# Kernel optimization log

Hardware: AMD Instinct MI355X
Metric: run time of the kernel (lower is better)

## Reference

```python
import jax, jax.numpy as jnp
import numpy as np

N_VOLS, N_PARTS = 4, 8          # hard-coded in GL.forward
B = N_VOLS * N_PARTS            # asserted batch size = 32
DIM, HID, PROJ = 8192, 4096, 256
TEMP = 0.1
BN_EPS = 1e-5


def setup_inputs() -> dict:
    key = jax.random.key(0)
    k = jax.random.split(key, 5)
    s1 = 1.0 / np.sqrt(DIM)
    s2 = 1.0 / np.sqrt(HID)
    return {
        "x": jax.random.normal(k[0], (B, DIM), jnp.float32),
        "W1": jax.random.uniform(k[1], (DIM, HID), jnp.float32, -s1, s1),
        "b1": jax.random.uniform(k[2], (HID,), jnp.float32, -s1, s1),
        "gamma": jnp.ones((HID,), jnp.float32),
        "beta": jnp.zeros((HID,), jnp.float32),
        "W2": jax.random.uniform(k[3], (HID, PROJ), jnp.float32, -s2, s2),
        "b2": jax.random.uniform(k[4], (PROJ,), jnp.float32, -s2, s2),
    }


def _gl_loss(proj):
    # F.normalize(p=2, dim=-1); CosineSimilarity on unit vectors == dot product
    p = proj / jnp.linalg.norm(proj, axis=-1, keepdims=True)
    sims = (p @ p.T) / TEMP                       # [B, B]
    idx = jnp.arange(B)
    # pos_index(i) = {i % n_parts + v * n_parts} -> same part id; includes i itself
    pos_mask = (idx[:, None] % N_PARTS) == (idx[None, :] % N_PARTS)  # [B, B], 4 per row
    neg_mask = ~pos_mask                                             # 28 per row
    E = jnp.exp(sims)                              # original uses raw exp (no max-shift)
    row_neg = jnp.sum(jnp.where(neg_mask, E, 0.0), axis=1)    # sum_j exp(s[i, neg_j])
    ET = E.T                                        # ET[i, p] = exp(s[p, i])
    col_neg = jnp.sum(jnp.where(neg_mask, ET, 0.0), axis=1)   # sum_j exp(s[neg_j, i])
    t1 = -jnp.log(E / (E + row_neg[:, None]))      # row-direction term per (i, pos)
    t2 = -jnp.log(ET / (ET + col_neg[:, None]))    # column-direction term per (i, pos)
    per_row = jnp.sum(jnp.where(pos_mask, t1 + t2, 0.0), axis=1) / N_VOLS
    return jnp.sum(per_row) / (B * 2)


def reference(x, W1, b1, gamma, beta, W2, b2):
    # projector MLP: Linear -> BatchNorm1d (training stats) -> ReLU -> Linear
    h = x @ W1 + b1
    mu = jnp.mean(h, axis=0)
    var = jnp.var(h, axis=0)                       # biased variance, BN training mode
    h = gamma * (h - mu) * jax.lax.rsqrt(var + BN_EPS) + beta
    h = jax.nn.relu(h)
    proj = h @ W2 + b2                             # [B, PROJ]
    return _gl_loss(proj)
```

## Files before the change

### kernel.cpp

```cpp
#include <hip/hip_runtime.h>

#define DIM   8192
#define HID   4096
#define PROJ  256
#define NB    32
#define KSPLIT 8
#define KCH   (DIM / KSPLIT)

typedef __attribute__((ext_vector_type(8))) short bf16x8;
typedef __attribute__((ext_vector_type(4))) float f32x4;

__device__ __forceinline__ float bf2f(unsigned short u) {
    return __uint_as_float(((unsigned)u) << 16);
}
__device__ __forceinline__ unsigned short f2bf(float f) {
    unsigned u = __float_as_uint(f);
    u += 0x7fffu + ((u >> 16) & 1u);
    return (unsigned short)(u >> 16);
}
__device__ __forceinline__ unsigned pk2(float a, float b) {
    return (unsigned)f2bf(a) | ((unsigned)f2bf(b) << 16);
}

__device__ __forceinline__ bool detect_bf16(const unsigned* __restrict__ xw, int lane) {
    unsigned v = xw[lane];
    int e = (int)((v >> 7) & 0xffu);
    bool pl = (e >= 100 && e <= 135);
    unsigned long long b = __ballot(pl);
    return __popcll(b) >= 32;
}

__global__ __launch_bounds__(256, 2) void gemm1_kernel(
    const void* __restrict__ xv, const void* __restrict__ W1v,
    float* __restrict__ hpart)
{
    __shared__ unsigned short wt[2 * 32 * 66];
    const int t  = threadIdx.x;
    const int nb = blockIdx.x & 63;
    const int kc = blockIdx.x >> 6;
    const int n0 = nb * 64;
    const int k0 = kc * KCH;

    const bool isbf = detect_bf16((const unsigned*)xv, t & 63);
    const unsigned short* xu  = (const unsigned short*)xv;
    const float*          xf  = (const float*)xv;
    const unsigned short* W1u = (const unsigned short*)W1v;
    const float*          W1f = (const float*)W1v;

    const int lane = t & 63;
    const int w    = t >> 6;
    const int g    = lane >> 4;
    const int ln   = lane & 15;
    const int wr   = t >> 3;
    const int wc   = (t & 7) * 8;

    auto loadW1 = [&](int kt) -> uint4 {
        const int base = (k0 + kt * 32 + wr) * HID + n0 + wc;
        if (isbf) return *(const uint4*)(W1u + base);
        float4 f0 = *(const float4*)(W1f + base);
        float4 f1 = *(const float4*)(W1f + base + 4);
        return make_uint4(pk2(f0.x, f0.y), pk2(f0.z, f0.w),
                          pk2(f1.x, f1.y), pk2(f1.z, f1.w));
    };
    auto storeTile = [&](int buf, uint4 v) {
        unsigned* dst = (unsigned*)&wt[buf * 2112 + wr * 66 + wc];
        dst[0] = v.x; dst[1] = v.y; dst[2] = v.z; dst[3] = v.w;
    };
    auto loadA = [&](int kt, int mt) -> bf16x8 {
        const int base = (mt * 16 + ln) * DIM + k0 + kt * 32 + g * 8;
        if (isbf) return *(const bf16x8*)(xu + base);
        float4 f0 = *(const float4*)(xf + base);
        float4 f1 = *(const float4*)(xf + base + 4);
        union { uint4 u; bf16x8 v; } c;
        c.u = make_uint4(pk2(f0.x, f0.y), pk2(f0.z, f0.w),
                         pk2(f1.x, f1.y), pk2(f1.z, f1.w));
        return c.v;
    };

    storeTile(0, loadW1(0));
    bf16x8 a0 = loadA(0, 0);
    bf16x8 a1 = loadA(0, 1);
    uint4  p0 = loadW1(1);
    __syncthreads();

    f32x4 acc0 = {0.f, 0.f, 0.f, 0.f};
    f32x4 acc1 = {0.f, 0.f, 0.f, 0.f};
    const int bco = w * 16 + ln;

    for (int kt = 0; kt < 32; ++kt) {
        const int cur = kt & 1;
        uint4 p1 = p0;
        if (kt + 2 < 32) p1 = loadW1(kt + 2);
        bf16x8 na0 = a0, na1 = a1;
        if (kt + 1 < 32) { na0 = loadA(kt + 1, 0); na1 = loadA(kt + 1, 1); }

        bf16x8 b;
        const unsigned short* wpb = wt + cur * 2112 + g * 528 + bco;
        #pragma unroll
        for (int j = 0; j < 8; ++j) b[j] = (short)wpb[j * 66];

        acc0 = __builtin_amdgcn_mfma_f32_16x16x32_bf16(a0, b, acc0, 0, 0, 0);
        acc1 = __builtin_amdgcn_mfma_f32_16x16x32_bf16(a1, b, acc1, 0, 0, 0);

        if (kt + 1 < 32) storeTile(cur ^ 1, p0);
        __syncthreads();
        p0 = p1; a0 = na0; a1 = na1;
    }

    const int col = n0 + w * 16 + ln;
    #pragma unroll
    for (int r = 0; r < 4; ++r) {
        hpart[(kc * NB + g * 4 + r) * HID + col]      = acc0[r];
        hpart[(kc * NB + 16 + g * 4 + r) * HID + col] = acc1[r];
    }
}

__global__ __launch_bounds__(256) void transpose_kernel(
    const void* __restrict__ W2v, unsigned short* __restrict__ W2T,
    const void* __restrict__ xv)
{
    __shared__ unsigned short tile[64][72];
    const int t  = threadIdx.x;
    const int bk = blockIdx.x & 63;
    const int bp = blockIdx.x >> 6;
    const bool isbf = detect_bf16((const unsigned*)xv, t & 63);
    const unsigned short* W2u = (const unsigned short*)W2v;
    const float*          W2f = (const float*)W2v;

    #pragma unroll
    for (int i = 0; i < 2; ++i) {
        int c  = i * 256 + t;
        int r  = c >> 3;
        int c8 = (c & 7) * 8;
        int base = (bk * 64 + r) * PROJ + bp * 64 + c8;
        unsigned u0, u1, u2, u3;
        if (isbf) {
            uint4 v = *(const uint4*)(W2u + base);
            u0 = v.x; u1 = v.y; u2 = v.z; u3 = v.w;
        } else {
            float4 f0 = *(const float4*)(W2f + base);
            float4 f1 = *(const float4*)(W2f + base + 4);
            u0 = pk2(f0.x, f0.y); u1 = pk2(f0.z, f0.w);
            u2 = pk2(f1.x, f1.y); u3 = pk2(f1.z, f1.w);
        }
        unsigned* dst = (unsigned*)&tile[r][c8];
        dst[0] = u0; dst[1] = u1; dst[2] = u2; dst[3] = u3;
    }
    __syncthreads();
    #pragma unroll
    for (int i = 0; i < 2; ++i) {
        int c  = i * 256 + t;
        int p  = c >> 3;
        int k8 = (c & 7) * 8;
        unsigned short tmp[8];
        #pragma unroll
        for (int j = 0; j < 8; ++j) tmp[j] = tile[k8 + j][p];
        uint4 v;
        v.x = (unsigned)tmp[0] | ((unsigned)tmp[1] << 16);
        v.y = (unsigned)tmp[2] | ((unsigned)tmp[3] << 16);
        v.z = (unsigned)tmp[4] | ((unsigned)tmp[5] << 16);
        v.w = (unsigned)tmp[6] | ((unsigned)tmp[7] << 16);
        *(uint4*)(W2T + (bp * 64 + p) * HID + bk * 64 + k8) = v;
    }
}

__global__ __launch_bounds__(64) void bn_kernel(
    const float* __restrict__ hpart, const void* __restrict__ b1v,
    const void* __restrict__ gv, const void* __restrict__ bev,
    float* __restrict__ hrelu, const void* __restrict__ xv)
{
    const int t = threadIdx.x;
    const int n = blockIdx.x * 64 + t;
    const bool isbf = detect_bf16((const unsigned*)xv, t & 63);

    float h[NB];
    #pragma unroll
    for (int m = 0; m < NB; ++m) h[m] = 0.f;
    for (int kc = 0; kc < KSPLIT; ++kc) {
        #pragma unroll
        for (int m = 0; m < NB; ++m) h[m] += hpart[(kc * NB + m) * HID + n];
    }
    const float bb = isbf ? bf2f(((const unsigned short*)b1v)[n]) : ((const float*)b1v)[n];
    float mu = 0.f;
    #pragma unroll
    for (int m = 0; m < NB; ++m) { h[m] += bb; mu += h[m]; }
    mu *= (1.f / 32.f);
    float var = 0.f;
    #pragma unroll
    for (int m = 0; m < NB; ++m) { float d = h[m] - mu; var += d * d; }
    var *= (1.f / 32.f);
    const float ga = isbf ? bf2f(((const unsigned short*)gv)[n])  : ((const float*)gv)[n];
    const float be = isbf ? bf2f(((const unsigned short*)bev)[n]) : ((const float*)bev)[n];
    const float sc = ga * rsqrtf(var + 1e-5f);
    #pragma unroll
    for (int m = 0; m < NB; ++m) {
        float v = (h[m] - mu) * sc + be;
        hrelu[m * HID + n] = fmaxf(v, 0.f);
    }
}

__global__ __launch_bounds__(256) void gemm2_kernel(
    const float* __restrict__ hrelu, const unsigned short* __restrict__ W2T,
    const void* __restrict__ b2v, float* __restrict__ proj,
    const void* __restrict__ xv)
{
    const int t  = threadIdx.x;
    const int p0 = blockIdx.x * 2;
    float acc[64];
    #pragma unroll
    for (int i = 0; i < 64; ++i) acc[i] = 0.f;

    for (int j = 0; j < 16; ++j) {
        const int k = j * 256 + t;
        const float w0 = bf2f(W2T[p0 * HID + k]);
        const float w1 = bf2f(W2T[(p0 + 1) * HID + k]);
        #pragma unroll
        for (int m = 0; m < NB; ++m) {
            const float hv = hrelu[m * HID + k];
            acc[m * 2]     += hv * w0;
            acc[m * 2 + 1] += hv * w1;
        }
    }
    #pragma unroll
    for (int i = 0; i < 64; ++i) {
        #pragma unroll
        for (int s = 1; s < 64; s <<= 1) acc[i] += __shfl_xor(acc[i], s);
    }
    __shared__ float red[4][64];
    const int wv = t >> 6, lane = t & 63;
    if (lane == 0) {
        #pragma unroll
        for (int i = 0; i < 64; ++i) red[wv][i] = acc[i];
    }
    __syncthreads();
    if (t < 64) {
        const float s = red[0][t] + red[1][t] + red[2][t] + red[3][t];
        const int m = t >> 1, pp = t & 1;
        const bool isbf = detect_bf16((const unsigned*)xv, t & 63);
        const float b2 = isbf ? bf2f(((const unsigned short*)b2v)[p0 + pp])
                              : ((const float*)b2v)[p0 + pp];
        proj[m * PROJ + p0 + pp] = s + b2;
    }
}

__global__ __launch_bounds__(256) void loss_part_kernel(
    const float* __restrict__ proj, float* __restrict__ rowtot)
{
    __shared__ float ps[32][260];
    __shared__ float npart[32][8];
    __shared__ float inrm[32];
    const int t = threadIdx.x;

    #pragma unroll
    for (int i = 0; i < 8; ++i) {
        int c  = i * 256 + t;
        int r  = c >> 6;
        int c4 = (c & 63) * 4;
        float4 v = *(const float4*)(proj + r * PROJ + c4);
        *(float4*)&ps[r][c4] = v;
    }
    __syncthreads();
    {
        const int r = t >> 3, seg = t & 7;
        float s = 0.f;
        #pragma unroll
        for (int c = 0; c < 32; ++c) { float v = ps[r][seg * 32 + c]; s += v * v; }
        npart[r][seg] = s;
    }
    __syncthreads();
    if (t < 32) {
        float s = 0.f;
        #pragma unroll
        for (int j = 0; j < 8; ++j) s += npart[t][j];
        inrm[t] = rsqrtf(s);
    }
    __syncthreads();

    const int li   = t >> 6;
    const int i    = blockIdx.x * 4 + li;
    const int j    = (t >> 1) & 31;
    const int half = t & 1;
    float acc = 0.f;
    const int cb = half * 128;
    #pragma unroll
    for (int c = 0; c < 128; c += 4) {
        float4 a = *(const float4*)&ps[i][cb + c];
        float4 b = *(const float4*)&ps[j][cb + c];
        acc += a.x * b.x + a.y * b.y + a.z * b.z + a.w * b.w;
    }
    acc += __shfl_xor(acc, 1);

    const float sim = acc * inrm[i] * inrm[j] * 10.0f;
    const float E   = __expf(sim);
    const bool pos  = ((j & 7) == (i & 7));

    float nv = (!pos && half == 0) ? E : 0.f;
    #pragma unroll
    for (int s = 1; s < 64; s <<= 1) nv += __shfl_xor(nv, s);
    float pv = (pos && half == 0) ? (logf(E + nv) - sim) : 0.f;
    #pragma unroll
    for (int s = 1; s < 64; s <<= 1) pv += __shfl_xor(pv, s);
    if ((t & 63) == 0) rowtot[i] = pv;
}

__global__ __launch_bounds__(64) void loss_final_kernel(
    const float* __restrict__ rowtot, unsigned* __restrict__ out)
{
    const int t = threadIdx.x;
    float v = (t < 32) ? rowtot[t] : 0.f;
    #pragma unroll
    for (int s = 1; s < 64; s <<= 1) v += __shfl_xor(v, s);
    if (t == 0) {
        const float loss = v * (1.0f / 128.0f);
        const unsigned lb = (unsigned)f2bf(loss);
        const unsigned base = (__float_as_uint(loss) & 0xffff0000u) | lb;
        unsigned best = base;
        float ebest = fabsf(__uint_as_float(base) - loss);
        const unsigned cp = base + 0x10000u;
        const float ep = fabsf(__uint_as_float(cp) - loss);
        if (ep < ebest) { best = cp; ebest = ep; }
        const unsigned cm = base - 0x10000u;
        const float em = fabsf(__uint_as_float(cm) - loss);
        if (em < ebest) { best = cm; }
        out[0] = best;
    }
}

extern "C" void kernel_launch(void* const* d_in, const int* in_sizes, int n_in,
                              void* d_out, int out_size, void* d_ws, size_t ws_size,
                              hipStream_t stream) {
    const void* x  = d_in[0];
    const void* W1 = d_in[1];
    const void* b1 = d_in[2];
    const void* ga = d_in[3];
    const void* be = d_in[4];
    const void* W2 = d_in[5];
    const void* b2 = d_in[6];

    char* wsp = (char*)d_ws;
    float* hpart = (float*)wsp;               wsp += (size_t)KSPLIT * NB * HID * 4;
    float* hrelu = (float*)wsp;               wsp += (size_t)NB * HID * 4;
    unsigned short* W2T = (unsigned short*)wsp; wsp += (size_t)PROJ * HID * 2;
    float* proj = (float*)wsp;                wsp += (size_t)NB * PROJ * 4;
    float* rowtot = (float*)wsp;              wsp += 32 * 4;

    gemm1_kernel<<<512, 256, 0, stream>>>(x, W1, hpart);
    transpose_kernel<<<256, 256, 0, stream>>>(W2, W2T, x);
    bn_kernel<<<64, 64, 0, stream>>>(hpart, b1, ga, be, hrelu, x);
    gemm2_kernel<<<128, 256, 0, stream>>>(hrelu, W2T, b2, proj, x);
    loss_part_kernel<<<8, 256, 0, stream>>>(proj, rowtot);
    loss_final_kernel<<<1, 64, 0, stream>>>(rowtot, (unsigned*)d_out);
}
```

Measured before the change: 263.9 us.

## Deepen GEMM1 split-K pipeline, MFMA GEMM2 on raw W2, fuse BN and loss kernels

Raises GEMM1 split-K to 16 with a three-deep W1 prefetch and double-buffered A registers, and drops the b1 add since batch-norm mean subtraction cancels it. Replaces the W2 transpose and scalar GEMM2 with an MFMA split-K kernel reading W2 directly from a bf16 hidden activation. Parallelizes BN statistics across threads, and merges the two loss kernels into one block that also reduces the GEMM2 partials. This is meant to cut launch count, the slow scalar projection GEMM, and memory-latency stalls, at the cost of larger split-K partial buffers and bf16 rounding of the hidden activations.

```diff
diff --git a/kernel.cpp b/kernel.cpp
--- a/kernel.cpp
+++ b/kernel.cpp
@@ -4,8 +4,12 @@
 #define HID   4096
 #define PROJ  256
 #define NB    32
-#define KSPLIT 8
-#define KCH   (DIM / KSPLIT)
+#define KSP1  16
+#define KCH1  (DIM / KSP1)
+#define KT1   (KCH1 / 32)
+#define KSP2  16
+#define KCH2  (HID / KSP2)
+#define KT2   (KCH2 / 32)
 
 typedef __attribute__((ext_vector_type(8))) short bf16x8;
 typedef __attribute__((ext_vector_type(4))) float f32x4;
@@ -30,7 +34,7 @@
     return __popcll(b) >= 32;
 }
 
-__global__ __launch_bounds__(256, 2) void gemm1_kernel(
+__global__ __launch_bounds__(256, 4) void gemm1_kernel(
     const void* __restrict__ xv, const void* __restrict__ W1v,
     float* __restrict__ hpart)
 {
@@ -39,7 +43,7 @@
     const int nb = blockIdx.x & 63;
     const int kc = blockIdx.x >> 6;
     const int n0 = nb * 64;
-    const int k0 = kc * KCH;
+    const int k0 = kc * KCH1;
 
     const bool isbf = detect_bf16((const unsigned*)xv, t & 63);
     const unsigned short* xu  = (const unsigned short*)xv;
@@ -78,36 +82,35 @@
     };
 
     storeTile(0, loadW1(0));
-    bf16x8 a0 = loadA(0, 0);
-    bf16x8 a1 = loadA(0, 1);
-    uint4  p0 = loadW1(1);
+    uint4 pf[3];
+    pf[0] = loadW1(1); pf[1] = loadW1(2); pf[2] = loadW1(3);
+    bf16x8 areg[2][2];
+    areg[0][0] = loadA(0, 0); areg[0][1] = loadA(0, 1);
+    areg[1][0] = loadA(1, 0); areg[1][1] = loadA(1, 1);
     __syncthreads();
 
     f32x4 acc0 = {0.f, 0.f, 0.f, 0.f};
     f32x4 acc1 = {0.f, 0.f, 0.f, 0.f};
     const int bco = w * 16 + ln;
 
-    for (int kt = 0; kt < 32; ++kt) {
+    #pragma unroll
+    for (int kt = 0; kt < KT1; ++kt) {
         const int cur = kt & 1;
-        uint4 p1 = p0;
-        if (kt + 2 < 32) p1 = loadW1(kt + 2);
-        bf16x8 na0 = a0, na1 = a1;
-        if (kt + 1 < 32) { na0 = loadA(kt + 1, 0); na1 = loadA(kt + 1, 1); }
-
         bf16x8 b;
-        const unsigned short* wpb = wt + cur * 2112 + g * 528 + bco;
+        const unsigned short* wpb = &wt[cur * 2112 + g * 528 + bco];
         #pragma unroll
         for (int j = 0; j < 8; ++j) b[j] = (short)wpb[j * 66];
 
-        acc0 = __builtin_amdgcn_mfma_f32_16x16x32_bf16(a0, b, acc0, 0, 0, 0);
-        acc1 = __builtin_amdgcn_mfma_f32_16x16x32_bf16(a1, b, acc1, 0, 0, 0);
-
-        if (kt + 1 < 32) storeTile(cur ^ 1, p0);
+        acc0 = __builtin_amdgcn_mfma_f32_16x16x32_bf16(areg[cur][0], b, acc0, 0, 0, 0);
+        acc1 = __builtin_amdgcn_mfma_f32_16x16x32_bf16(areg[cur][1], b, acc1, 0, 0, 0);
+
+        if (kt + 2 < KT1) { areg[cur][0] = loadA(kt + 2, 0); areg[cur][1] = loadA(kt + 2, 1); }
+        if (kt + 1 < KT1) storeTile(cur ^ 1, pf[kt % 3]);
+        if (kt + 4 < KT1) pf[kt % 3] = loadW1(kt + 4);
         __syncthreads();
-        p0 = p1; a0 = na0; a1 = na1;
-    }
-
-    const int col = n0 + w * 16 + ln;
+    }
+
+    const int col = n0 + bco;
     #pragma unroll
     for (int r = 0; r < 4; ++r) {
         hpart[(kc * NB + g * 4 + r) * HID + col]      = acc0[r];
@@ -115,214 +118,218 @@
     }
 }
 
-__global__ __launch_bounds__(256) void transpose_kernel(
-    const void* __restrict__ W2v, unsigned short* __restrict__ W2T,
+__global__ __launch_bounds__(256) void bnrelu_kernel(
+    const float* __restrict__ hpart, const void* __restrict__ gv,
+    const void* __restrict__ bev, unsigned short* __restrict__ hrelu,
     const void* __restrict__ xv)
 {
-    __shared__ unsigned short tile[64][72];
+    const int t = threadIdx.x;
+    const int c = t & 15, q = t >> 4;
+    const int n = blockIdx.x * 16 + c;
+    const bool isbf = detect_bf16((const unsigned*)xv, t & 63);
+
+    float h0 = 0.f, h1 = 0.f;
+    #pragma unroll
+    for (int kc = 0; kc < KSP1; ++kc) {
+        h0 += hpart[(kc * NB + 2 * q) * HID + n];
+        h1 += hpart[(kc * NB + 2 * q + 1) * HID + n];
+    }
+
+    __shared__ float red[16][16];
+    __shared__ float stat[2][16];
+    red[q][c] = h0 + h1;
+    __syncthreads();
+    if (t < 16) {
+        float s = 0.f;
+        #pragma unroll
+        for (int i = 0; i < 16; ++i) s += red[i][t];
+        stat[0][t] = s * (1.f / 32.f);
+    }
+    __syncthreads();
+    const float mu = stat[0][c];
+    const float d0 = h0 - mu, d1 = h1 - mu;
+    red[q][c] = d0 * d0 + d1 * d1;
+    __syncthreads();
+    if (t < 16) {
+        float v = 0.f;
+        #pragma unroll
+        for (int i = 0; i < 16; ++i) v += red[i][t];
+        v *= (1.f / 32.f);
+        const int nn = blockIdx.x * 16 + t;
+        const float ga = isbf ? bf2f(((const unsigned short*)gv)[nn])  : ((const float*)gv)[nn];
+        const float be = isbf ? bf2f(((const unsigned short*)bev)[nn]) : ((const float*)bev)[nn];
+        stat[0][t] = ga * rsqrtf(v + 1e-5f);
+        stat[1][t] = be;
+    }
+    __syncthreads();
+    const float sc = stat[0][c], be = stat[1][c];
+    hrelu[(2 * q) * HID + n]     = f2bf(fmaxf(d0 * sc + be, 0.f));
+    hrelu[(2 * q + 1) * HID + n] = f2bf(fmaxf(d1 * sc + be, 0.f));
+}
+
+__global__ __launch_bounds__(256, 4) void gemm2_kernel(
+    const unsigned short* __restrict__ hrelu, const void* __restrict__ W2v,
+    float* __restrict__ ppart, const void* __restrict__ xv)
+{
+    __shared__ unsigned short wt[2 * 32 * 66];
     const int t  = threadIdx.x;
-    const int bk = blockIdx.x & 63;
-    const int bp = blockIdx.x >> 6;
+    const int nb = blockIdx.x & 3;
+    const int kc = blockIdx.x >> 2;
+    const int n0 = nb * 64;
+    const int k0 = kc * KCH2;
+
     const bool isbf = detect_bf16((const unsigned*)xv, t & 63);
     const unsigned short* W2u = (const unsigned short*)W2v;
     const float*          W2f = (const float*)W2v;
 
-    #pragma unroll
-    for (int i = 0; i < 2; ++i) {
-        int c  = i * 256 + t;
-        int r  = c >> 3;
-        int c8 = (c & 7) * 8;
-        int base = (bk * 64 + r) * PROJ + bp * 64 + c8;
-        unsigned u0, u1, u2, u3;
-        if (isbf) {
-            uint4 v = *(const uint4*)(W2u + base);
-            u0 = v.x; u1 = v.y; u2 = v.z; u3 = v.w;
-        } else {
-            float4 f0 = *(const float4*)(W2f + base);
-            float4 f1 = *(const float4*)(W2f + base + 4);
-            u0 = pk2(f0.x, f0.y); u1 = pk2(f0.z, f0.w);
-            u2 = pk2(f1.x, f1.y); u3 = pk2(f1.z, f1.w);
-        }
-        unsigned* dst = (unsigned*)&tile[r][c8];
-        dst[0] = u0; dst[1] = u1; dst[2] = u2; dst[3] = u3;
-    }
-    __syncthreads();
-    #pragma unroll
-    for (int i = 0; i < 2; ++i) {
-        int c  = i * 256 + t;
-        int p  = c >> 3;
-        int k8 = (c & 7) * 8;
-        unsigned short tmp[8];
-        #pragma unroll
-        for (int j = 0; j < 8; ++j) tmp[j] = tile[k8 + j][p];
-        uint4 v;
-        v.x = (unsigned)tmp[0] | ((unsigned)tmp[1] << 16);
-        v.y = (unsigned)tmp[2] | ((unsigned)tmp[3] << 16);
-        v.z = (unsigned)tmp[4] | ((unsigned)tmp[5] << 16);
-        v.w = (unsigned)tmp[6] | ((unsigned)tmp[7] << 16);
-        *(uint4*)(W2T + (bp * 64 + p) * HID + bk * 64 + k8) = v;
-    }
-}
-
-__global__ __launch_bounds__(64) void bn_kernel(
-    const float* __restrict__ hpart, const void* __restrict__ b1v,
-    const void* __restrict__ gv, const void* __restrict__ bev,
-    float* __restrict__ hrelu, const void* __restrict__ xv)
-{
-    const int t = threadIdx.x;
-    const int n = blockIdx.x * 64 + t;
-    const bool isbf = detect_bf16((const unsigned*)xv, t & 63);
-
-    float h[NB];
-    #pragma unroll
-    for (int m = 0; m < NB; ++m) h[m] = 0.f;
-    for (int kc = 0; kc < KSPLIT; ++kc) {
-        #pragma unroll
-        for (int m = 0; m < NB; ++m) h[m] += hpart[(kc * NB + m) * HID + n];
-    }
-    const float bb = isbf ? bf2f(((const unsigned short*)b1v)[n]) : ((const float*)b1v)[n];
-    float mu = 0.f;
-    #pragma unroll
-    for (int m = 0; m < NB; ++m) { h[m] += bb; mu += h[m]; }
-    mu *= (1.f / 32.f);
-    float var = 0.f;
-    #pragma unroll
-    for (int m = 0; m < NB; ++m) { float d = h[m] - mu; var += d * d; }
-    var *= (1.f / 32.f);
-    const float ga = isbf ? bf2f(((const unsigned short*)gv)[n])  : ((const float*)gv)[n];
-    const float be = isbf ? bf2f(((const unsigned short*)bev)[n]) : ((const float*)bev)[n];
-    const float sc = ga * rsqrtf(var + 1e-5f);
-    #pragma unroll
-    for (int m = 0; m < NB; ++m) {
-        float v = (h[m] - mu) * sc + be;
-        hrelu[m * HID + n] = fmaxf(v, 0.f);
-    }
-}
-
-__global__ __launch_bounds__(256) void gemm2_kernel(
-    const float* __restrict__ hrelu, const unsigned short* __restrict__ W2T,
-    const void* __restrict__ b2v, float* __restrict__ proj,
-    const void* __restrict__ xv)
-{
-    const int t  = threadIdx.x;
-    const int p0 = blockIdx.x * 2;
-    float acc[64];
-    #pragma unroll
-    for (int i = 0; i < 64; ++i) acc[i] = 0.f;
-
-    for (int j = 0; j < 16; ++j) {
-        const int k = j * 256 + t;
-        const float w0 = bf2f(W2T[p0 * HID + k]);
-        const float w1 = bf2f(W2T[(p0 + 1) * HID + k]);
-        #pragma unroll
-        for (int m = 0; m < NB; ++m) {
-            const float hv = hrelu[m * HID + k];
-            acc[m * 2]     += hv * w0;
-            acc[m * 2 + 1] += hv * w1;
-        }
-    }
-    #pragma unroll
-    for (int i = 0; i < 64; ++i) {
-        #pragma unroll
-        for (int s = 1; s < 64; s <<= 1) acc[i] += __shfl_xor(acc[i], s);
-    }
-    __shared__ float red[4][64];
-    const int wv = t >> 6, lane = t & 63;
-    if (lane == 0) {
-        #pragma unroll
-        for (int i = 0; i < 64; ++i) red[wv][i] = acc[i];
-    }
-    __syncthreads();
-    if (t < 64) {
-        const float s = red[0][t] + red[1][t] + red[2][t] + red[3][t];
-        const int m = t >> 1, pp = t & 1;
-        const bool isbf = detect_bf16((const unsigned*)xv, t & 63);
-        const float b2 = isbf ? bf2f(((const unsigned short*)b2v)[p0 + pp])
-                              : ((const float*)b2v)[p0 + pp];
-        proj[m * PROJ + p0 + pp] = s + b2;
-    }
-}
-
-__global__ __launch_bounds__(256) void loss_part_kernel(
-    const float* __restrict__ proj, float* __restrict__ rowtot)
+    const int lane = t & 63;
+    const int w    = t >> 6;
+    const int g    = lane >> 4;
+    const int ln   = lane & 15;
+    const int wr   = t >> 3;
+    const int wc   = (t & 7) * 8;
+
+    auto loadW2 = [&](int kt) -> uint4 {
+        const int base = (k0 + kt * 32 + wr) * PROJ + n0 + wc;
+        if (isbf) return *(const uint4*)(W2u + base);
+        float4 f0 = *(const float4*)(W2f + base);
+        float4 f1 = *(const float4*)(W2f + base + 4);
+        return make_uint4(pk2(f0.x, f0.y), pk2(f0.z, f0.w),
+                          pk2(f1.x, f1.y), pk2(f1.z, f1.w));
+    };
+    auto storeTile = [&](int buf, uint4 v) {
+        unsigned* dst = (unsigned*)&wt[buf * 2112 + wr * 66 + wc];
+        dst[0] = v.x; dst[1] = v.y; dst[2] = v.z; dst[3] = v.w;
+    };
+    auto loadA = [&](int kt, int mt) -> bf16x8 {
+        return *(const bf16x8*)(hrelu + (mt * 16 + ln) * HID + k0 + kt * 32 + g * 8);
+    };
+
+    storeTile(0, loadW2(0));
+    uint4 pf[3];
+    pf[0] = loadW2(1); pf[1] = loadW2(2); pf[2] = loadW2(3);
+    bf16x8 areg[2][2];
+    areg[0][0] = loadA(0, 0); areg[0][1] = loadA(0, 1);
+    areg[1][0] = loadA(1, 0); areg[1][1] = loadA(1, 1);
+    __syncthreads();
+
+    f32x4 acc0 = {0.f, 0.f, 0.f, 0.f};
+    f32x4 acc1 = {0.f, 0.f, 0.f, 0.f};
+    const int bco = w * 16 + ln;
+
+    #pragma unroll
+    for (int kt = 0; kt < KT2; ++kt) {
+        const int cur = kt & 1;
+        bf16x8 b;
+        const unsigned short* wpb = &wt[cur * 2112 + g * 528 + bco];
+        #pragma unroll
+        for (int j = 0; j < 8; ++j) b[j] = (short)wpb[j * 66];
+
+        acc0 = __builtin_amdgcn_mfma_f32_16x16x32_bf16(areg[cur][0], b, acc0, 0, 0, 0);
+        acc1 = __builtin_amdgcn_mfma_f32_16x16x32_bf16(areg[cur][1], b, acc1, 0, 0, 0);
+
+        if (kt + 2 < KT2) { areg[cur][0] = loadA(kt + 2, 0); areg[cur][1] = loadA(kt + 2, 1); }
+        if (kt + 1 < KT2) storeTile(cur ^ 1, pf[kt % 3]);
+        if (kt + 4 < KT2) pf[kt % 3] = loadW2(kt + 4);
+        __syncthreads();
+    }
+
+    const int col = n0 + bco;
+    #pragma unroll
+    for (int r = 0; r < 4; ++r) {
+        ppart[(kc * NB + g * 4 + r) * PROJ + col]      = acc0[r];
+        ppart[(kc * NB + 16 + g * 4 + r) * PROJ + col] = acc1[r];
+    }
+}
+
+__global__ __launch_bounds__(1024) void loss_kernel(
+    const float* __restrict__ ppart, const void* __restrict__ b2v,
+    const void* __restrict__ xv, unsigned* __restrict__ out)
 {
     __shared__ float ps[32][260];
-    __shared__ float npart[32][8];
+    __shared__ float npart2[32][8];
     __shared__ float inrm[32];
+    __shared__ float rowtot[32];
     const int t = threadIdx.x;
+    const bool isbf = detect_bf16((const unsigned*)xv, t & 63);
 
     #pragma unroll
     for (int i = 0; i < 8; ++i) {
-        int c  = i * 256 + t;
-        int r  = c >> 6;
-        int c4 = (c & 63) * 4;
-        float4 v = *(const float4*)(proj + r * PROJ + c4);
-        *(float4*)&ps[r][c4] = v;
-    }
-    __syncthreads();
-    {
+        const int o = i * 1024 + t;
+        float s = 0.f;
+        #pragma unroll
+        for (int s16 = 0; s16 < KSP2; ++s16) s += ppart[s16 * (NB * PROJ) + o];
+        const int c = o & 255;
+        s += isbf ? bf2f(((const unsigned short*)b2v)[c]) : ((const float*)b2v)[c];
+        ps[o >> 8][c] = s;
+    }
+    __syncthreads();
+
+    if (t < 256) {
         const int r = t >> 3, seg = t & 7;
         float s = 0.f;
         #pragma unroll
         for (int c = 0; c < 32; ++c) { float v = ps[r][seg * 32 + c]; s += v * v; }
-        npart[r][seg] = s;
+        npart2[r][seg] = s;
     }
     __syncthreads();
     if (t < 32) {
         float s = 0.f;
         #pragma unroll
-        for (int j = 0; j < 8; ++j) s += npart[t][j];
+        for (int j = 0; j < 8; ++j) s += npart2[t][j];
         inrm[t] = rsqrtf(s);
     }
     __syncthreads();
 
-    const int li   = t >> 6;
-    const int i    = blockIdx.x * 4 + li;
-    const int j    = (t >> 1) & 31;
-    const int half = t & 1;
-    float acc = 0.f;
-    const int cb = half * 128;
-    #pragma unroll
-    for (int c = 0; c < 128; c += 4) {
-        float4 a = *(const float4*)&ps[i][cb + c];
-        float4 b = *(const float4*)&ps[j][cb + c];
-        acc += a.x * b.x + a.y * b.y + a.z * b.z + a.w * b.w;
-    }
-    acc += __shfl_xor(acc, 1);
-
-    const float sim = acc * inrm[i] * inrm[j] * 10.0f;
-    const float E   = __expf(sim);
-    const bool pos  = ((j & 7) == (i & 7));
-
-    float nv = (!pos && half == 0) ? E : 0.f;
-    #pragma unroll
-    for (int s = 1; s < 64; s <<= 1) nv += __shfl_xor(nv, s);
-    float pv = (pos && half == 0) ? (logf(E + nv) - sim) : 0.f;
-    #pragma unroll
-    for (int s = 1; s < 64; s <<= 1) pv += __shfl_xor(pv, s);
-    if ((t & 63) == 0) rowtot[i] = pv;
-}
-
-__global__ __launch_bounds__(64) void loss_final_kernel(
-    const float* __restrict__ rowtot, unsigned* __restrict__ out)
-{
-    const int t = threadIdx.x;
-    float v = (t < 32) ? rowtot[t] : 0.f;
-    #pragma unroll
-    for (int s = 1; s < 64; s <<= 1) v += __shfl_xor(v, s);
-    if (t == 0) {
-        const float loss = v * (1.0f / 128.0f);
-        const unsigned lb = (unsigned)f2bf(loss);
-        const unsigned base = (__float_as_uint(loss) & 0xffff0000u) | lb;
-        unsigned best = base;
-        float ebest = fabsf(__uint_as_float(base) - loss);
-        const unsigned cp = base + 0x10000u;
-        const float ep = fabsf(__uint_as_float(cp) - loss);
-        if (ep < ebest) { best = cp; ebest = ep; }
-        const unsigned cm = base - 0x10000u;
-        const float em = fabsf(__uint_as_float(cm) - loss);
-        if (em < ebest) { best = cm; }
-        out[0] = best;
+    const int wv   = t >> 6;
+    const int lane = t & 63;
+    const int j    = (lane >> 1) & 31;
+    const int half = lane & 1;
+    #pragma unroll
+    for (int rr = 0; rr < 2; ++rr) {
+        const int i = wv * 2 + rr;
+        float acc = 0.f;
+        const int cb = half * 128;
+        #pragma unroll
+        for (int c = 0; c < 128; c += 4) {
+            float4 a = *(const float4*)&ps[i][cb + c];
+            float4 b = *(const float4*)&ps[j][cb + c];
+            acc += a.x * b.x + a.y * b.y + a.z * b.z + a.w * b.w;
+        }
+        acc += __shfl_xor(acc, 1);
+
+        const float sim = acc * inrm[i] * inrm[j] * 10.0f;
+        const float E   = __expf(sim);
+        const bool pos  = ((j & 7) == (i & 7));
+
+        float nv = (!pos && half == 0) ? E : 0.f;
+        #pragma unroll
+        for (int s = 1; s < 64; s <<= 1) nv += __shfl_xor(nv, s);
+        float pv = (pos && half == 0) ? (logf(E + nv) - sim) : 0.f;
+        #pragma unroll
+        for (int s = 1; s < 64; s <<= 1) pv += __shfl_xor(pv, s);
+        if (lane == 0) rowtot[i] = pv;
+    }
+    __syncthreads();
+
+    if (t < 64) {
+        float v = (t < 32) ? rowtot[t] : 0.f;
+        #pragma unroll
+        for (int s = 1; s < 64; s <<= 1) v += __shfl_xor(v, s);
+        if (t == 0) {
+            const float loss = v * (1.0f / 128.0f);
+            const unsigned lb = (unsigned)f2bf(loss);
+            const unsigned base = (__float_as_uint(loss) & 0xffff0000u) | lb;
+            unsigned best = base;
+            float ebest = fabsf(__uint_as_float(base) - loss);
+            const unsigned cp = base + 0x10000u;
+            const float ep = fabsf(__uint_as_float(cp) - loss);
+            if (ep < ebest) { best = cp; ebest = ep; }
+            const unsigned cm = base - 0x10000u;
+            const float em = fabsf(__uint_as_float(cm) - loss);
+            if (em < ebest) { best = cm; }
+            out[0] = best;
+        }
     }
 }
 
@@ -331,23 +338,18 @@
                               hipStream_t stream) {
     const void* x  = d_in[0];
     const void* W1 = d_in[1];
-    const void* b1 = d_in[2];
     const void* ga = d_in[3];
     const void* be = d_in[4];
     const void* W2 = d_in[5];
     const void* b2 = d_in[6];
 
     char* wsp = (char*)d_ws;
-    float* hpart = (float*)wsp;               wsp += (size_t)KSPLIT * NB * HID * 4;
-    float* hrelu = (float*)wsp;               wsp += (size_t)NB * HID * 4;
-    unsigned short* W2T = (unsigned short*)wsp; wsp += (size_t)PROJ * HID * 2;
-    float* proj = (float*)wsp;                wsp += (size_t)NB * PROJ * 4;
-    float* rowtot = (float*)wsp;              wsp += 32 * 4;
-
-    gemm1_kernel<<<512, 256, 0, stream>>>(x, W1, hpart);
-    transpose_kernel<<<256, 256, 0, stream>>>(W2, W2T, x);
-    bn_kernel<<<64, 64, 0, stream>>>(hpart, b1, ga, be, hrelu, x);
-    gemm2_kernel<<<128, 256, 0, stream>>>(hrelu, W2T, b2, proj, x);
-    loss_part_kernel<<<8, 256, 0, stream>>>(proj, rowtot);
-    loss_final_kernel<<<1, 64, 0, stream>>>(rowtot, (unsigned*)d_out);
-}
+    float* hpart = (float*)wsp;                 wsp += (size_t)KSP1 * NB * HID * 4;
+    unsigned short* hrelu = (unsigned short*)wsp; wsp += (size_t)NB * HID * 2;
+    float* ppart = (float*)wsp;                 wsp += (size_t)KSP2 * NB * PROJ * 4;
+
+    gemm1_kernel<<<1024, 256, 0, stream>>>(x, W1, hpart);
+    bnrelu_kernel<<<256, 256, 0, stream>>>(hpart, ga, be, hrelu, x);
+    gemm2_kernel<<<64, 256, 0, stream>>>(hrelu, W2, ppart, x);
+    loss_kernel<<<1, 1024, 0, stream>>>(ppart, b2, x, (unsigned*)d_out);
+}
```

Result: faster. 243.8 us (-7.6%).
